# Kernel optimization log

Measured on AMD Instinct MI355X. Metric: run time of the kernel, lower is better.

Reference implementation:

```python
import jax, jax.numpy as jnp
import numpy as np

S, N, B, EMB = 20, 102400, 1024, 64


def setup_inputs() -> dict:
    key = jax.random.key(0)
    ks = jax.random.split(key, 8)
    nodes_abs = jax.random.normal(ks[0], (S, N, 2), jnp.float32) * 5.0
    nodes_norm = jax.random.normal(ks[1], (S, N, 2), jnp.float32)
    shift_value = jax.random.normal(ks[2], (S, N, 2), jnp.float32)
    seq_list = jax.random.uniform(ks[3], (S, N), jnp.float32) - 0.02
    scenes = jnp.arange(B, dtype=jnp.int32)
    pednum = jnp.full((B,), N // B, dtype=jnp.int32)  # peds per scene
    # TSModel stand-in parameters (2 -> EMB -> 2 with GM-history mixing)
    W_in = jax.random.normal(ks[4], (2, EMB), jnp.float32) * 0.5
    W_gm = jax.random.normal(ks[5], (EMB, EMB), jnp.float32) * (1.0 / np.sqrt(EMB))
    b_h = jnp.zeros((EMB,), jnp.float32)
    W_out = jax.random.normal(ks[6], (EMB, 2), jnp.float32) * (1.0 / np.sqrt(EMB))
    b_out = jnp.zeros((2,), jnp.float32)
    return {"nodes_abs": nodes_abs, "nodes_norm": nodes_norm, "shift_value": shift_value,
            "seq_list": seq_list, "scenes": scenes, "pednum": pednum,
            "W_in": W_in, "W_gm": W_gm, "b_h": b_h, "W_out": W_out, "b_out": b_out}


def reference(nodes_abs, nodes_norm, shift_value, seq_list, scenes, pednum,
              W_in, W_gm, b_h, W_out, b_out):
    S_, N_, _ = nodes_abs.shape
    B_ = pednum.shape[0]
    # scene id per pedestrian from cumsum(pednum) -- replaces get_st_ed slices
    scene_ids = jnp.searchsorted(jnp.cumsum(pednum), jnp.arange(N_), side="right")
    presence = seq_list > 0

    def step(carry, xs):
        mask, gm_sum = carry            # mask: [N] peds present in all frames 0..f
        pres_f, abs_f, f = xs
        mask = mask & pres_f            # get_node_index(seq_list[:f+1])
        mf = mask.astype(abs_f.dtype)   # [N]
        # center_alignment_spa: per-scene mean over active peds at frame f
        cnt = jax.ops.segment_sum(mf, scene_ids, num_segments=B_)
        ssum = jax.ops.segment_sum(abs_f * mf[:, None], scene_ids, num_segments=B_)
        center = ssum / jnp.maximum(cnt, 1.0)[:, None]            # [B,2]
        coord = (abs_f - center[scene_ids]) * mf[:, None]         # [N,2]
        # TSModel stand-in: embed centered coord + running GM-history mean
        gm_mean = gm_sum / jnp.maximum(f, 1).astype(gm_sum.dtype)  # mean of GM[:f]
        h = jnp.tanh(coord @ W_in + gm_mean @ W_gm + b_h) * mf[:, None]  # [N,EMB]
        out = (h @ W_out + b_out) * mf[:, None]                    # masked scatter write
        return (mask, gm_sum + h), out

    mask0 = jnp.ones((N_,), dtype=bool)
    gm0 = jnp.zeros((N_, W_gm.shape[0]), nodes_abs.dtype)
    xs = (presence[: S_ - 1], nodes_abs[: S_ - 1], jnp.arange(S_ - 1))
    _, outs = jax.lax.scan(step, (mask0, gm0), xs)                # [S-1,N,2]
    outputs = jnp.concatenate([outs, jnp.zeros((1, N_, 2), outs.dtype)], axis=0)
    return outputs
```

## Files before the change

kernel.cpp:

```cpp
#include <hip/hip_runtime.h>

#define S_DIM 20
#define EMB   64
#define GSTR  36

typedef __attribute__((ext_vector_type(8))) short bf16x8;
typedef __attribute__((ext_vector_type(4))) float f32x4;

__device__ __forceinline__ uint32_t pk_bf16(float lo, float hi) {
    uint32_t r;
    asm("v_cvt_pk_bf16_f32 %0, %1, %2" : "=v"(r) : "v"(lo), "v"(hi));
    return r;
}
__device__ __forceinline__ short bf16s(float v) {
    return (short)(pk_bf16(v, v) & 0xffffu);
}
__device__ __forceinline__ float unbf16(uint32_t lo16) {
    union { uint32_t u; float f; } c; c.u = lo16 << 16; return c.f;
}

__global__ __launch_bounds__(512, 2) void pfa_kernel(
    const float* __restrict__ nodes_abs,
    const float* __restrict__ seq_list,
    const int*   __restrict__ pednum,
    const float* __restrict__ W_in,
    const float* __restrict__ W_gm,
    const float* __restrict__ b_h,
    const float* __restrict__ W_out,
    const float* __restrict__ b_out,
    float*       __restrict__ out,
    int N, int B)
{
    const int b    = blockIdx.x;
    const int t    = threadIdx.x;
    const int lane = t & 63;
    const int w    = t >> 6;
    const int l15  = lane & 15;
    const int hi   = lane >> 4;

    __shared__ uint32_t G[8 * 16 * GSTR];
    uint32_t* const Gw = &G[w * 16 * GSTR];

    int partial = 0;
    for (int i = lane; i < b; i += 64) partial += pednum[i];
    #pragma unroll
    for (int off = 32; off; off >>= 1) partial += __shfl_xor(partial, off, 64);
    const int start = partial;
    const int P = min(pednum[b], 128);
    const int q = (P + 7) >> 3;

    for (int i = lane; i < 16 * GSTR; i += 64) Gw[i] = 0;

    bf16x8 agm[4][2];
    #pragma unroll
    for (int m = 0; m < 4; ++m)
        #pragma unroll
        for (int T = 0; T < 2; ++T)
            #pragma unroll
            for (int e = 0; e < 8; ++e)
                agm[m][T][e] = bf16s(W_gm[(32*T + 8*hi + e) * EMB + 16*m + l15]);

    bf16x8 aaug[4];
    #pragma unroll
    for (int m = 0; m < 4; ++m) {
        bf16x8 a = {0,0,0,0,0,0,0,0};
        if (hi == 0) {
            const int j = 16*m + l15;
            const float w0 = W_in[j], w1 = W_in[EMB + j], bh = b_h[j];
            const short w0h = bf16s(w0); const short w0l = bf16s(w0 - unbf16((uint16_t)w0h));
            const short w1h = bf16s(w1); const short w1l = bf16s(w1 - unbf16((uint16_t)w1h));
            const short bhh = bf16s(bh); const short bhl = bf16s(bh - unbf16((uint16_t)bhh));
            a[0]=w0h; a[1]=w0l; a[2]=w0h; a[3]=w1h; a[4]=w1l; a[5]=w1h; a[6]=bhh; a[7]=bhl;
        }
        aaug[m] = a;
    }

    f32x4 wo0[4], wo1[4];
    #pragma unroll
    for (int m = 0; m < 4; ++m)
        #pragma unroll
        for (int r = 0; r < 4; ++r) {
            const float2 v = *(const float2*)&W_out[(16*m + 4*hi + r) * 2];
            wo0[m][r] = v.x; wo1[m][r] = v.y;
        }
    const float bo0 = b_out[0], bo1 = b_out[1];

    const int  pA = lane, pB = lane + 64, pR = w * q + l15;
    const bool vA = pA < P, vB = pB < P;
    const bool vR = (l15 < q) && (pR < P);
    const int  iA = start + (vA ? pA : 0);
    const int  iB = start + (vB ? pB : 0);
    const int  iR = start + (vR ? pR : 0);

    float  seqA = seq_list[iA], seqB = seq_list[iB], seqR = seq_list[iR];
    float2 absA = *(const float2*)&nodes_abs[(size_t)iA * 2];
    float2 absB = *(const float2*)&nodes_abs[(size_t)iB * 2];
    float2 absR = *(const float2*)&nodes_abs[(size_t)iR * 2];

    bool aliveA = true, aliveB = true, aliveR = true;
    f32x4 gm[4];
    const f32x4 zero4 = {0.f, 0.f, 0.f, 0.f};
    #pragma unroll
    for (int m = 0; m < 4; ++m) gm[m] = zero4;

    #pragma unroll 1
    for (int f = 0; f < S_DIM - 1; ++f) {
        aliveA = aliveA && (seqA > 0.0f);
        aliveB = aliveB && (seqB > 0.0f);
        aliveR = aliveR && (seqR > 0.0f);
        const float mfA = (aliveA && vA) ? 1.0f : 0.0f;
        const float mfB = (aliveB && vB) ? 1.0f : 0.0f;
        const float mfR = (aliveR && vR) ? 1.0f : 0.0f;
        float cnt = mfA + mfB;
        float sx  = fmaf(absA.x, mfA, absB.x * mfB);
        float sy  = fmaf(absA.y, mfA, absB.y * mfB);
        const float axR = absR.x, ayR = absR.y;

        const size_t nb = (size_t)(f + 1) * N;
        const float  nseqA = seq_list[nb + iA], nseqB = seq_list[nb + iB], nseqR = seq_list[nb + iR];
        const float2 nabsA = *(const float2*)&nodes_abs[(nb + iA) * 2];
        const float2 nabsB = *(const float2*)&nodes_abs[(nb + iB) * 2];
        const float2 nabsR = *(const float2*)&nodes_abs[(nb + iR) * 2];

        #pragma unroll
        for (int off = 32; off; off >>= 1) {
            cnt += __shfl_xor(cnt, off, 64);
            sx  += __shfl_xor(sx , off, 64);
            sy  += __shfl_xor(sy , off, 64);
        }
        const float inv_c = __builtin_amdgcn_rcpf(fmaxf(cnt, 1.0f));
        const float cx = sx * inv_c, cy = sy * inv_c;
        const float cxd = axR - cx, cyd = ayR - cy;

        const uint32_t e0 = pk_bf16(cxd, cxd);
        const float    cxl = cxd - unbf16(e0 & 0xffffu);
        const uint32_t ey = pk_bf16(cyd, cyd);
        const float    cyl = cyd - unbf16(ey & 0xffffu);
        const uint32_t e1 = pk_bf16(cxl, cyd);
        const uint32_t e2 = pk_bf16(cyd, cyl);
        union { uint32_t u[4]; bf16x8 v; } b2u;
        const bool h0 = (hi == 0);
        b2u.u[0] = h0 ? e0 : 0u;
        b2u.u[1] = h0 ? e1 : 0u;
        b2u.u[2] = h0 ? e2 : 0u;
        b2u.u[3] = h0 ? 0x3f803f80u : 0u;

        const bf16x8 B0 = *(const bf16x8*)&Gw[l15 * GSTR +      4*hi];
        const bf16x8 B1 = *(const bf16x8*)&Gw[l15 * GSTR + 16 + 4*hi];

        f32x4 acc[4];
        #pragma unroll
        for (int m = 0; m < 4; ++m) {
            f32x4 c = zero4;
            c = __builtin_amdgcn_mfma_f32_16x16x32_bf16(aaug[m],   b2u.v, c, 0, 0, 0);
            c = __builtin_amdgcn_mfma_f32_16x16x32_bf16(agm[m][0], B0,    c, 0, 0, 0);
            c = __builtin_amdgcn_mfma_f32_16x16x32_bf16(agm[m][1], B1,    c, 0, 0, 0);
            acc[m] = c;
        }

        const float m2 = -2.0f * mfR;
        float o0 = 0.0f, o1 = 0.0f;
        f32x4 h[4];
        #pragma unroll
        for (int m = 0; m < 4; ++m) {
            #pragma unroll
            for (int r = 0; r < 4; ++r) {
                const float x  = acc[m][r];
                const float e  = __expf(2.0f * x);
                const float tt = __builtin_amdgcn_rcpf(e + 1.0f);
                const float hv = fmaf(tt, m2, mfR);
                h[m][r] = hv;
                o0 = fmaf(hv, wo0[m][r], o0);
                o1 = fmaf(hv, wo1[m][r], o1);
            }
            gm[m] += h[m];
        }
        o0 += __shfl_xor(o0, 16, 64);  o0 += __shfl_xor(o0, 32, 64);
        o1 += __shfl_xor(o1, 16, 64);  o1 += __shfl_xor(o1, 32, 64);
        if (h0 && vR) {
            float2 o;
            o.x = (o0 + bo0) * mfR;
            o.y = (o1 + bo1) * mfR;
            *(float2*)&out[((size_t)f * N + iR) * 2] = o;
        }

        const float invf2 = __builtin_amdgcn_rcpf((float)(f + 1));
        #pragma unroll
        for (int m = 0; m < 4; ++m) {
            const uint32_t p0 = pk_bf16(gm[m][0] * invf2, gm[m][1] * invf2);
            const uint32_t p1 = pk_bf16(gm[m][2] * invf2, gm[m][3] * invf2);
            *(uint2*)&Gw[l15 * GSTR + 8*m + 2*hi] = make_uint2(p0, p1);
        }

        seqA = nseqA; seqB = nseqB; seqR = nseqR;
        absA = nabsA; absB = nabsB; absR = nabsR;
    }

    if (t < P) {
        const size_t o = ((size_t)(S_DIM - 1) * N + start + t) * 2;
        out[o] = 0.0f; out[o + 1] = 0.0f;
    }
}

extern "C" void kernel_launch(void* const* d_in, const int* in_sizes, int n_in,
                              void* d_out, int out_size, void* d_ws, size_t ws_size,
                              hipStream_t stream) {
    const float* nodes_abs = (const float*)d_in[0];
    const float* seq_list  = (const float*)d_in[3];
    const int*   pednum    = (const int*)  d_in[5];
    const float* W_in      = (const float*)d_in[6];
    const float* W_gm      = (const float*)d_in[7];
    const float* b_h       = (const float*)d_in[8];
    const float* W_out     = (const float*)d_in[9];
    const float* b_out     = (const float*)d_in[10];
    float*       out       = (float*)d_out;

    const int N = in_sizes[3] / S_DIM;
    const int B = in_sizes[5];

    pfa_kernel<<<B, 512, 0, stream>>>(nodes_abs, seq_list, pednum,
                                      W_in, W_gm, b_h, W_out, b_out,
                                      out, N, B);
}
```

Baseline: 100.6 us.

## Precompute masks and scene centers up front, halve block size, MFMA output projection

Presence masks are now computed once into shared memory as bitmasks, and per-frame scene centers are computed ahead of time by waves in parallel. This removes the per-step cross-lane reductions and the redundant seq_list loads from the sequential loop. Blocks shrink to 256 threads, with each wave handling two 16-pedestrian tiles in the recurrence. The output projection moves from scalar FMAs plus shuffles to an MFMA over bf16 h values staged in LDS, which adds LDS traffic and some bf16 rounding on the output path.

```diff
diff --git a/kernel.cpp b/kernel.cpp
--- a/kernel.cpp
+++ b/kernel.cpp
@@ -1,8 +1,10 @@
 #include <hip/hip_runtime.h>
 
 #define S_DIM 20
+#define NSTEP 19
 #define EMB   64
-#define GSTR  36
+#define GSTR  72
+#define MAXP  128
 
 typedef __attribute__((ext_vector_type(8))) short bf16x8;
 typedef __attribute__((ext_vector_type(4))) float f32x4;
@@ -12,14 +14,12 @@
     asm("v_cvt_pk_bf16_f32 %0, %1, %2" : "=v"(r) : "v"(lo), "v"(hi));
     return r;
 }
-__device__ __forceinline__ short bf16s(float v) {
-    return (short)(pk_bf16(v, v) & 0xffffu);
-}
+__device__ __forceinline__ short bf16s(float v) { return (short)(pk_bf16(v, v) & 0xffffu); }
 __device__ __forceinline__ float unbf16(uint32_t lo16) {
     union { uint32_t u; float f; } c; c.u = lo16 << 16; return c.f;
 }
 
-__global__ __launch_bounds__(512, 2) void pfa_kernel(
+__global__ __launch_bounds__(256, 4) void pfa_kernel(
     const float* __restrict__ nodes_abs,
     const float* __restrict__ seq_list,
     const int*   __restrict__ pednum,
@@ -38,18 +38,23 @@
     const int l15  = lane & 15;
     const int hi   = lane >> 4;
 
-    __shared__ uint32_t G[8 * 16 * GSTR];
-    uint32_t* const Gw = &G[w * 16 * GSTR];
+    __shared__ __attribute__((aligned(16))) uint32_t G[8 * 16 * GSTR];
+    __shared__ uint32_t masks[MAXP];
+    __shared__ float2   cxy[NSTEP];
 
     int partial = 0;
     for (int i = lane; i < b; i += 64) partial += pednum[i];
     #pragma unroll
     for (int off = 32; off; off >>= 1) partial += __shfl_xor(partial, off, 64);
     const int start = partial;
-    const int P = min(pednum[b], 128);
+    const int P = min(pednum[b], MAXP);
     const int q = (P + 7) >> 3;
 
-    for (int i = lane; i < 16 * GSTR; i += 64) Gw[i] = 0;
+    {
+        uint4* g4 = (uint4*)&G[(w * 2) * 16 * GSTR];
+        for (int i = lane; i < 2 * 16 * GSTR / 4; i += 64)
+            g4[i] = make_uint4(0u, 0u, 0u, 0u);
+    }
 
     bf16x8 agm[4][2];
     #pragma unroll
@@ -75,125 +80,143 @@
         aaug[m] = a;
     }
 
-    f32x4 wo0[4], wo1[4];
-    #pragma unroll
-    for (int m = 0; m < 4; ++m)
-        #pragma unroll
-        for (int r = 0; r < 4; ++r) {
-            const float2 v = *(const float2*)&W_out[(16*m + 4*hi + r) * 2];
-            wo0[m][r] = v.x; wo1[m][r] = v.y;
+    bf16x8 aout[2];
+    #pragma unroll
+    for (int T = 0; T < 2; ++T)
+        #pragma unroll
+        for (int e = 0; e < 8; ++e) {
+            const int j = 32*T + 8*hi + e;
+            aout[T][e] = (l15 < 2) ? bf16s(W_out[j*2 + l15]) : (short)0;
         }
     const float bo0 = b_out[0], bo1 = b_out[1];
 
-    const int  pA = lane, pB = lane + 64, pR = w * q + l15;
-    const bool vA = pA < P, vB = pB < P;
-    const bool vR = (l15 < q) && (pR < P);
-    const int  iA = start + (vA ? pA : 0);
-    const int  iB = start + (vB ? pB : 0);
-    const int  iR = start + (vR ? pR : 0);
-
-    float  seqA = seq_list[iA], seqB = seq_list[iB], seqR = seq_list[iR];
-    float2 absA = *(const float2*)&nodes_abs[(size_t)iA * 2];
-    float2 absB = *(const float2*)&nodes_abs[(size_t)iB * 2];
-    float2 absR = *(const float2*)&nodes_abs[(size_t)iR * 2];
-
-    bool aliveA = true, aliveB = true, aliveR = true;
-    f32x4 gm[4];
-    const f32x4 zero4 = {0.f, 0.f, 0.f, 0.f};
-    #pragma unroll
-    for (int m = 0; m < 4; ++m) gm[m] = zero4;
-
-    #pragma unroll 1
-    for (int f = 0; f < S_DIM - 1; ++f) {
-        aliveA = aliveA && (seqA > 0.0f);
-        aliveB = aliveB && (seqB > 0.0f);
-        aliveR = aliveR && (seqR > 0.0f);
-        const float mfA = (aliveA && vA) ? 1.0f : 0.0f;
-        const float mfB = (aliveB && vB) ? 1.0f : 0.0f;
-        const float mfR = (aliveR && vR) ? 1.0f : 0.0f;
-        float cnt = mfA + mfB;
-        float sx  = fmaf(absA.x, mfA, absB.x * mfB);
-        float sy  = fmaf(absA.y, mfA, absB.y * mfB);
-        const float axR = absR.x, ayR = absR.y;
-
-        const size_t nb = (size_t)(f + 1) * N;
-        const float  nseqA = seq_list[nb + iA], nseqB = seq_list[nb + iB], nseqR = seq_list[nb + iR];
-        const float2 nabsA = *(const float2*)&nodes_abs[(nb + iA) * 2];
-        const float2 nabsB = *(const float2*)&nodes_abs[(nb + iB) * 2];
-        const float2 nabsR = *(const float2*)&nodes_abs[(nb + iR) * 2];
-
+    if (t < P) {
+        uint32_t m = 0; bool alive = true;
+        #pragma unroll
+        for (int f = 0; f < NSTEP; ++f) {
+            alive = alive && (seq_list[(size_t)f * N + start + t] > 0.0f);
+            m |= (alive ? 1u : 0u) << f;
+        }
+        masks[t] = m;
+    }
+    __syncthreads();
+
+    for (int f = w; f < NSTEP; f += 4) {
+        float cnt = 0.f, sx = 0.f, sy = 0.f;
+        for (int p = lane; p < P; p += 64) {
+            const float mf = (float)((masks[p] >> f) & 1u);
+            const float2 a = *(const float2*)&nodes_abs[((size_t)f * N + start + p) * 2];
+            cnt += mf; sx = fmaf(a.x, mf, sx); sy = fmaf(a.y, mf, sy);
+        }
         #pragma unroll
         for (int off = 32; off; off >>= 1) {
             cnt += __shfl_xor(cnt, off, 64);
             sx  += __shfl_xor(sx , off, 64);
             sy  += __shfl_xor(sy , off, 64);
         }
-        const float inv_c = __builtin_amdgcn_rcpf(fmaxf(cnt, 1.0f));
-        const float cx = sx * inv_c, cy = sy * inv_c;
-        const float cxd = axR - cx, cyd = ayR - cy;
-
-        const uint32_t e0 = pk_bf16(cxd, cxd);
-        const float    cxl = cxd - unbf16(e0 & 0xffffu);
-        const uint32_t ey = pk_bf16(cyd, cyd);
-        const float    cyl = cyd - unbf16(ey & 0xffffu);
-        const uint32_t e1 = pk_bf16(cxl, cyd);
-        const uint32_t e2 = pk_bf16(cyd, cyl);
-        union { uint32_t u[4]; bf16x8 v; } b2u;
-        const bool h0 = (hi == 0);
-        b2u.u[0] = h0 ? e0 : 0u;
-        b2u.u[1] = h0 ? e1 : 0u;
-        b2u.u[2] = h0 ? e2 : 0u;
-        b2u.u[3] = h0 ? 0x3f803f80u : 0u;
-
-        const bf16x8 B0 = *(const bf16x8*)&Gw[l15 * GSTR +      4*hi];
-        const bf16x8 B1 = *(const bf16x8*)&Gw[l15 * GSTR + 16 + 4*hi];
-
-        f32x4 acc[4];
-        #pragma unroll
-        for (int m = 0; m < 4; ++m) {
-            f32x4 c = zero4;
-            c = __builtin_amdgcn_mfma_f32_16x16x32_bf16(aaug[m],   b2u.v, c, 0, 0, 0);
-            c = __builtin_amdgcn_mfma_f32_16x16x32_bf16(agm[m][0], B0,    c, 0, 0, 0);
-            c = __builtin_amdgcn_mfma_f32_16x16x32_bf16(agm[m][1], B1,    c, 0, 0, 0);
-            acc[m] = c;
-        }
-
-        const float m2 = -2.0f * mfR;
-        float o0 = 0.0f, o1 = 0.0f;
-        f32x4 h[4];
-        #pragma unroll
-        for (int m = 0; m < 4; ++m) {
-            #pragma unroll
-            for (int r = 0; r < 4; ++r) {
-                const float x  = acc[m][r];
-                const float e  = __expf(2.0f * x);
-                const float tt = __builtin_amdgcn_rcpf(e + 1.0f);
-                const float hv = fmaf(tt, m2, mfR);
-                h[m][r] = hv;
-                o0 = fmaf(hv, wo0[m][r], o0);
-                o1 = fmaf(hv, wo1[m][r], o1);
-            }
-            gm[m] += h[m];
-        }
-        o0 += __shfl_xor(o0, 16, 64);  o0 += __shfl_xor(o0, 32, 64);
-        o1 += __shfl_xor(o1, 16, 64);  o1 += __shfl_xor(o1, 32, 64);
-        if (h0 && vR) {
-            float2 o;
-            o.x = (o0 + bo0) * mfR;
-            o.y = (o1 + bo1) * mfR;
-            *(float2*)&out[((size_t)f * N + iR) * 2] = o;
-        }
-
+        if (lane == 0) {
+            const float ic = __builtin_amdgcn_rcpf(fmaxf(cnt, 1.0f));
+            cxy[f] = make_float2(sx * ic, sy * ic);
+        }
+    }
+    __syncthreads();
+
+    bool     vr[2];
+    int      gi[2];
+    uint32_t mk[2];
+    float2   ab[2];
+    #pragma unroll
+    for (int r = 0; r < 2; ++r) {
+        const int pd = 2*q*w + r*q + l15;
+        vr[r] = (l15 < q) && (pd < P);
+        gi[r] = start + (vr[r] ? pd : 0);
+        mk[r] = vr[r] ? masks[pd] : 0u;
+        ab[r] = *(const float2*)&nodes_abs[(size_t)gi[r] * 2];
+    }
+
+    f32x4 gm[2][4];
+    const f32x4 zero4 = {0.f, 0.f, 0.f, 0.f};
+    #pragma unroll
+    for (int r = 0; r < 2; ++r)
+        #pragma unroll
+        for (int m = 0; m < 4; ++m) gm[r][m] = zero4;
+
+    const bool h0 = (hi == 0);
+
+    #pragma unroll 1
+    for (int f = 0; f < NSTEP; ++f) {
+        const float2 c = cxy[f];
         const float invf2 = __builtin_amdgcn_rcpf((float)(f + 1));
-        #pragma unroll
-        for (int m = 0; m < 4; ++m) {
-            const uint32_t p0 = pk_bf16(gm[m][0] * invf2, gm[m][1] * invf2);
-            const uint32_t p1 = pk_bf16(gm[m][2] * invf2, gm[m][3] * invf2);
-            *(uint2*)&Gw[l15 * GSTR + 8*m + 2*hi] = make_uint2(p0, p1);
-        }
-
-        seqA = nseqA; seqB = nseqB; seqR = nseqR;
-        absA = nabsA; absB = nabsB; absR = nabsR;
+
+        #pragma unroll
+        for (int r = 0; r < 2; ++r) {
+            uint32_t* const Grow = &G[((w*2 + r) * 16 + l15) * GSTR];
+            const float mf  = (float)((mk[r] >> f) & 1u);
+            const float cxd = ab[r].x - c.x;
+            const float cyd = ab[r].y - c.y;
+            ab[r] = *(const float2*)&nodes_abs[((size_t)(f + 1) * N + gi[r]) * 2];
+
+            const uint32_t e0 = pk_bf16(cxd, cxd);
+            const float    cxl = cxd - unbf16(e0 & 0xffffu);
+            const uint32_t ey = pk_bf16(cyd, cyd);
+            const float    cyl = cyd - unbf16(ey & 0xffffu);
+            const uint32_t e1 = pk_bf16(cxl, cyd);
+            const uint32_t e2 = pk_bf16(cyd, cyl);
+            union { uint32_t u[4]; bf16x8 v; } b2u;
+            b2u.u[0] = h0 ? e0 : 0u;
+            b2u.u[1] = h0 ? e1 : 0u;
+            b2u.u[2] = h0 ? e2 : 0u;
+            b2u.u[3] = h0 ? 0x3f803f80u : 0u;
+
+            const bf16x8 B0 = *(const bf16x8*)&Grow[ 0 + 4*hi];
+            const bf16x8 B1 = *(const bf16x8*)&Grow[16 + 4*hi];
+
+            f32x4 acc[4];
+            #pragma unroll
+            for (int m = 0; m < 4; ++m) {
+                f32x4 cacc = zero4;
+                cacc = __builtin_amdgcn_mfma_f32_16x16x32_bf16(aaug[m],   b2u.v, cacc, 0, 0, 0);
+                cacc = __builtin_amdgcn_mfma_f32_16x16x32_bf16(agm[m][0], B0,    cacc, 0, 0, 0);
+                cacc = __builtin_amdgcn_mfma_f32_16x16x32_bf16(agm[m][1], B1,    cacc, 0, 0, 0);
+                acc[m] = cacc;
+            }
+
+            const float m2 = -2.0f * mf;
+            #pragma unroll
+            for (int m = 0; m < 4; ++m) {
+                f32x4 h4;
+                #pragma unroll
+                for (int rr = 0; rr < 4; ++rr) {
+                    const float x  = acc[m][rr];
+                    const float e  = __expf(2.0f * x);
+                    const float tt = __builtin_amdgcn_rcpf(e + 1.0f);
+                    h4[rr] = fmaf(tt, m2, mf);
+                }
+                gm[r][m] += h4;
+                const uint32_t p0 = pk_bf16(h4[0], h4[1]);
+                const uint32_t p1 = pk_bf16(h4[2], h4[3]);
+                *(uint2*)&Grow[32 + 8*m + 2*hi] = make_uint2(p0, p1);
+            }
+
+            const bf16x8 H0 = *(const bf16x8*)&Grow[32 + 4*hi];
+            const bf16x8 H1 = *(const bf16x8*)&Grow[48 + 4*hi];
+            f32x4 oc = zero4;
+            oc = __builtin_amdgcn_mfma_f32_16x16x32_bf16(aout[0], H0, oc, 0, 0, 0);
+            oc = __builtin_amdgcn_mfma_f32_16x16x32_bf16(aout[1], H1, oc, 0, 0, 0);
+            if (h0 && vr[r]) {
+                float2 o;
+                o.x = (oc[0] + bo0) * mf;
+                o.y = (oc[1] + bo1) * mf;
+                *(float2*)&out[((size_t)f * N + gi[r]) * 2] = o;
+            }
+
+            #pragma unroll
+            for (int m = 0; m < 4; ++m) {
+                const uint32_t p0 = pk_bf16(gm[r][m][0] * invf2, gm[r][m][1] * invf2);
+                const uint32_t p1 = pk_bf16(gm[r][m][2] * invf2, gm[r][m][3] * invf2);
+                *(uint2*)&Grow[8*m + 2*hi] = make_uint2(p0, p1);
+            }
+        }
     }
 
     if (t < P) {
@@ -218,7 +241,7 @@
     const int N = in_sizes[3] / S_DIM;
     const int B = in_sizes[5];
 
-    pfa_kernel<<<B, 512, 0, stream>>>(nodes_abs, seq_list, pednum,
+    pfa_kernel<<<B, 256, 0, stream>>>(nodes_abs, seq_list, pednum,
                                       W_in, W_gm, b_h, W_out, b_out,
                                       out, N, B);
 }
```

Result: slower. 105.6 us (+5.0%).
